# Kernel tuning notes

Hardware: AMD Instinct MI355X
Metric: run time of the kernel (lower is better)

## Reference

```python
import jax, jax.numpy as jnp
import numpy as np


def setup_inputs() -> dict:
    key = jax.random.key(0)
    k1, k2, k3 = jax.random.split(key, 3)
    x = jax.random.normal(k1, (32, 256, 32, 32), dtype=jnp.float32)
    weight = jax.random.normal(k2, (256, 256, 3, 3), dtype=jnp.float32) * 0.05
    bias = jax.random.normal(k3, (256,), dtype=jnp.float32) * 0.01
    return {"x": x, "weight": weight, "bias": bias}


def _forward(x, weight, bias):
    B, cin, n, _ = x.shape
    cout, _, k, _ = weight.shape
    s = (k - 1) // 2
    nf = n // 2 + 1
    bins = n * nf

    # fft shift matrix: exp(-1j*2*pi*s*(i+j)/n), kept rfft columns
    idx = jnp.arange(n)
    shift = idx[None, :] + idx[:, None]                     # (n, n)
    shift_m = jnp.exp(-1j * 2 * jnp.pi * s * shift / n)[:, :nf]
    shift_m = shift_m.reshape(bins, 1, 1).astype(jnp.complex64)

    # xfft: (B, cin, n, nf) -> (bins, cin, B)
    xfft = jnp.fft.rfft2(x)
    xfft = jnp.transpose(xfft, (2, 3, 1, 0)).reshape(bins, cin, B)

    # Hfft: (cout, cin, n, nf) -> (bins, cout, cin), shifted + conj
    Hfft = jnp.fft.rfft2(weight, s=(n, n)).reshape(cout, cin, bins)
    Hfft = shift_m * jnp.conj(jnp.transpose(Hfft, (2, 0, 1)))

    def sq_abs(z):
        return jnp.real(z) ** 2 + jnp.imag(z) ** 2

    RowNorm = jnp.sqrt(jnp.sum(sq_abs(Hfft), axis=2))       # (bins, cout)
    ColNorm = jnp.sqrt(jnp.sum(sq_abs(Hfft), axis=1))       # (bins, cin)

    if cout >= cin:
        RowLoss = jnp.mean((RowNorm - jnp.sqrt(cin / cout)) ** 2)
        ColLoss = jnp.mean((ColNorm - 1.0) ** 2)
        HHT = jnp.einsum('npc,nqc->npq', jnp.conj(Hfft), Hfft)  # (bins, cout, cout)
        mask = jnp.triu(jnp.ones((cout, cout), bool), k=1)
        count = bins * (cout * (cout - 1) // 2)
        AngLoss = jnp.sum(sq_abs(HHT) * mask[None]) / count   # MSE(|HHT[triu]|, 0)
        L = cout * ColLoss + cin * RowLoss + AngLoss
    else:
        RowLoss = jnp.mean((RowNorm - 1.0) ** 2)
        ColLoss = jnp.mean((ColNorm - jnp.sqrt(cout / cin)) ** 2)
        HTH = jnp.einsum('ndp,ndq->npq', jnp.conj(Hfft), Hfft)  # (bins, cin, cin)
        mask = jnp.triu(jnp.ones((cin, cin), bool), k=1)
        count = bins * (cin * (cin - 1) // 2)
        AngLoss = jnp.sum(sq_abs(HTH) * mask[None]) / count
        L = cout * ColLoss + cin * RowLoss + AngLoss

    # per-bin complex matmul: (bins, cout, cin) @ (bins, cin, B) -> (bins, cout, B)
    yfft = Hfft @ xfft
    yfft = jnp.transpose(yfft.reshape(n, nf, cout, B), (3, 2, 0, 1))  # (B, cout, n, nf)
    y = jnp.fft.irfft2(yfft, s=(n, n))
    y = y + bias[None, :, None, None]
    return y, L


def reference(x, weight, bias):
    return _forward(x, weight, bias)
```

## Files before the change

kernel.cpp:

```cpp
#include <hip/hip_runtime.h>
#include <math.h>

typedef __attribute__((ext_vector_type(8)))  short  short8;
typedef __attribute__((ext_vector_type(16))) float  float16;

#define TWO_PI_OVER_32 0.19634954084936207f

static __device__ __forceinline__ unsigned short f2bf(float f) {
    unsigned int u = __float_as_uint(f);
    u = (u + 0x7FFFu + ((u >> 16) & 1u)) >> 16;
    return (unsigned short)u;
}
static __device__ __forceinline__ float bf2f(unsigned short s) {
    return __uint_as_float(((unsigned int)s) << 16);
}

static __device__ __forceinline__ void g2l16(const void* g, void* l) {
    __builtin_amdgcn_global_load_lds(
        (const __attribute__((address_space(1))) unsigned int*)g,
        (__attribute__((address_space(3))) unsigned int*)l, 16, 0, 0);
}

__global__ __launch_bounds__(256) void k_prepx(const float* __restrict__ x,
                                               unsigned short* __restrict__ xb,
                                               const float* __restrict__ w,
                                               unsigned short* __restrict__ wt,
                                               unsigned short* __restrict__ Vb,
                                               float* __restrict__ Drow,
                                               float* __restrict__ Dcol,
                                               float* __restrict__ accum) {
    int tid = threadIdx.x;
    if (blockIdx.x < 4096) {
        int g = blockIdx.x * 256 + tid;
        int c = g & 31, r = (g >> 5) & 31, cig = (g >> 10) & 31, b = g >> 15;
        const float* xp = x + ((b * 256 + cig * 8) * 32 + r) * 32 + c;
        union { unsigned short u[8]; uint4 v; } pk;
        #pragma unroll
        for (int u = 0; u < 8; ++u) pk.u[u] = f2bf(xp[u * 1024]);
        ((uint4*)xb)[g] = pk.v;
        return;
    }
    __shared__ float sdata[45];
    __shared__ float ws2[256 * 9];
    int blk = blockIdx.x - 4096, lane = tid & 63;
    bool colmode = blk >= 256;
    int pc = blk & 255;
    if (blk == 0 && tid < 4) accum[tid] = 0.f;
    if (tid < 45) sdata[tid] = 0.f;

    int p = colmode ? tid : pc;
    int c = colmode ? pc : tid;
    float w9[9];
    #pragma unroll
    for (int t = 0; t < 9; ++t) w9[t] = w[(p * 256 + c) * 9 + t];
    if (!colmode) {
        #pragma unroll
        for (int t = 0; t < 9; ++t) ws2[tid * 9 + t] = w9[t];
    }
    __syncthreads();

    int idx = 0;
    for (int ta = 0; ta < 9; ++ta)
        for (int tb = ta; tb < 9; ++tb) {
            float v = w9[ta] * w9[tb];
            #pragma unroll
            for (int off = 32; off > 0; off >>= 1) v += __shfl_down(v, off);
            if (lane == 0) atomicAdd(&sdata[idx], v);
            ++idx;
        }
    __syncthreads();
    if (tid < 45) (colmode ? Dcol : Drow)[pc * 45 + tid] = sdata[tid];

    if (!colmode) {
        #pragma unroll
        for (int t = 0; t < 9; ++t)
            wt[t * 65536 + (c >> 3) * 2048 + p * 8 + (c & 7)] = f2bf(w9[t]);
        if (tid < 320) {
            int ta = tid >> 5, cig = tid & 31;
            union { unsigned short u[8]; uint4 v; } pk;
            #pragma unroll
            for (int u = 0; u < 8; ++u)
                pk.u[u] = (ta < 9) ? f2bf(ws2[(cig * 8 + u) * 9 + ta]) : (unsigned short)0;
            ((uint4*)Vb)[(p * 10 + ta) * 32 + cig] = pk.v;
        }
    }
}

__global__ __launch_bounds__(256, 2) void k_conv(const unsigned short* __restrict__ xb,
                                                 const unsigned short* __restrict__ wt,
                                                 const float* __restrict__ bias,
                                                 float* __restrict__ y) {
    __shared__ unsigned short wsm[2][1152 * 8];

    const int tid  = threadIdx.x;
    const int lane = tid & 63;
    const int wv   = tid >> 6;
    const int half = lane >> 5;
    const int m    = lane & 31;

    const int id    = blockIdx.x;
    const int xcd   = id & 7;
    const int local = id >> 3;
    const int b     = xcd * 4 + (local >> 4);
    const int rem   = local & 15;
    const int co0   = (rem & 3) * 64;
    const int r0    = (rem >> 2) * 8;

    float16 acc[2][2];
    #pragma unroll
    for (int i = 0; i < 2; ++i)
        #pragma unroll
        for (int ns = 0; ns < 2; ++ns)
            #pragma unroll
            for (int r = 0; r < 16; ++r) acc[i][ns][r] = 0.f;

    const uint4*  wtv = (const uint4*)wt;
    const short8* xbg = (const short8*)xb;

    auto stage = [&](int buf, int kc) {
        uint4* dst = (uint4*)wsm[buf];
        #pragma unroll
        for (int wc = wv; wc < 18; wc += 4) {
            int t = wc >> 1, cig = wc & 1;
            g2l16(&wtv[t * 8192 + (kc * 2 + cig) * 256 + co0 + lane],
                  &dst[wc * 64]);
        }
    };

    stage(0, 0);
    int cur = 0;

    #pragma unroll 1
    for (int kc = 0; kc < 16; ++kc) {
        __syncthreads();

        short8 bfr[4][3];
        {
            const long cb = ((long)(b * 32 + kc * 2 + half) * 32) * 32;
            #pragma unroll
            for (int s = 0; s < 4; ++s) {
                int gr = (r0 + wv * 2 + s + 31) & 31;
                #pragma unroll
                for (int btv = 0; btv < 3; ++btv)
                    bfr[s][btv] = xbg[cb + gr * 32 + ((m + btv + 31) & 31)];
            }
        }
        if (kc < 15) stage(cur ^ 1, kc + 1);

        const short8* wsl = (const short8*)wsm[cur];
        #pragma unroll
        for (int t = 0; t < 9; ++t) {
            const int atv = t / 3, btv = t % 3;
            short8 a0 = wsl[(t * 2 + half) * 64 + m];
            short8 a1 = wsl[(t * 2 + half) * 64 + 32 + m];
            #pragma unroll
            for (int ns = 0; ns < 2; ++ns) {
                acc[0][ns] = __builtin_amdgcn_mfma_f32_32x32x16_bf16(a0, bfr[ns + atv][btv], acc[0][ns], 0, 0, 0);
                acc[1][ns] = __builtin_amdgcn_mfma_f32_32x32x16_bf16(a1, bfr[ns + atv][btv], acc[1][ns], 0, 0, 0);
            }
        }
        cur ^= 1;
    }

    #pragma unroll
    for (int i = 0; i < 2; ++i) {
        #pragma unroll
        for (int ns = 0; ns < 2; ++ns) {
            int r = r0 + wv * 2 + ns;
            #pragma unroll
            for (int reg = 0; reg < 16; ++reg) {
                int crow = (reg & 3) + 8 * (reg >> 2) + 4 * half;
                int co = co0 + i * 32 + crow;
                y[(b * 256 + co) * 1024 + r * 32 + m] = acc[i][ns][reg] + bias[co];
            }
        }
    }
}

__global__ __launch_bounds__(256) void k_gram(const unsigned short* __restrict__ Vb,
                                              unsigned short* __restrict__ Gb) {
    int blk = blockIdx.x, I = 0;
    while (blk >= 20 - I) { blk -= 20 - I; ++I; }
    int J = I + blk;

    const int tid  = threadIdx.x;
    const int lane = tid & 63;
    const int wave = tid >> 6;
    const int wm = wave >> 1, wn = wave & 1;
    const int half = lane >> 5;
    const int m = lane & 31;

    const int row0 = I * 128 + wm * 64;
    const int col0 = J * 128 + wn * 64;

    float16 acc[2][2];
    #pragma unroll
    for (int i = 0; i < 2; ++i)
        #pragma unroll
        for (int j = 0; j < 2; ++j)
            #pragma unroll
            for (int r = 0; r < 16; ++r) acc[i][j][r] = 0.f;

    const short8* vb = (const short8*)Vb;
    for (int kc = 0; kc < 16; ++kc) {
        int cig = kc * 2 + half;
        short8 a0 = vb[(row0 + m) * 32 + cig];
        short8 a1 = vb[(row0 + 32 + m) * 32 + cig];
        short8 b0 = vb[(col0 + m) * 32 + cig];
        short8 b1 = vb[(col0 + 32 + m) * 32 + cig];
        acc[0][0] = __builtin_amdgcn_mfma_f32_32x32x16_bf16(a0, b0, acc[0][0], 0, 0, 0);
        acc[0][1] = __builtin_amdgcn_mfma_f32_32x32x16_bf16(a0, b1, acc[0][1], 0, 0, 0);
        acc[1][0] = __builtin_amdgcn_mfma_f32_32x32x16_bf16(a1, b0, acc[1][0], 0, 0, 0);
        acc[1][1] = __builtin_amdgcn_mfma_f32_32x32x16_bf16(a1, b1, acc[1][1], 0, 0, 0);
    }
    #pragma unroll
    for (int i = 0; i < 2; ++i)
        #pragma unroll
        for (int j = 0; j < 2; ++j)
            #pragma unroll
            for (int reg = 0; reg < 16; ++reg) {
                int crow = (reg & 3) + 8 * (reg >> 2) + 4 * half;
                Gb[(row0 + i * 32 + crow) * 2560 + col0 + j * 32 + m] =
                    f2bf(acc[i][j][reg]);
            }
}

__global__ __launch_bounds__(256) void k_loss(const float* __restrict__ Drow,
                                              const float* __restrict__ Dcol,
                                              const unsigned short* __restrict__ Gb,
                                              float* __restrict__ accum) {
    __shared__ union {
        struct { float coef[45]; float red[2]; } rc;
        struct { unsigned short gs[9 * 2560]; float red; } ang;
    } sh;
    int tid = threadIdx.x;

    if (blockIdx.x < 544) {
        int bin = blockIdx.x;
        int u = bin / 17, v = bin % 17;
        if (tid < 2) sh.rc.red[tid] = 0.f;
        if (tid < 45) {
            int idx = 0, TA = 0, TB = 0;
            for (int ta = 0; ta < 9; ++ta)
                for (int tb = ta; tb < 9; ++tb) {
                    if (idx == tid) { TA = ta; TB = tb; }
                    ++idx;
                }
            int da = TA / 3 - TB / 3;
            int db = TA % 3 - TB % 3;
            float cth = cosf(TWO_PI_OVER_32 * (float)(u * da + v * db));
            sh.rc.coef[tid] = (TA == TB) ? 1.f : 2.f * cth;
        }
        __syncthreads();

        float s1 = 0.f, s2 = 0.f;
        const float* dr = Drow + tid * 45;
        const float* dc = Dcol + tid * 45;
        #pragma unroll
        for (int i = 0; i < 45; ++i) {
            s1 += sh.rc.coef[i] * dr[i];
            s2 += sh.rc.coef[i] * dc[i];
        }
        float e1 = sqrtf(fmaxf(s1, 0.f)) - 1.f; e1 *= e1;
        float e2 = sqrtf(fmaxf(s2, 0.f)) - 1.f; e2 *= e2;
        #pragma unroll
        for (int off = 32; off > 0; off >>= 1) {
            e1 += __shfl_down(e1, off);
            e2 += __shfl_down(e2, off);
        }
        if ((tid & 63) == 0) { atomicAdd(&sh.rc.red[0], e1); atomicAdd(&sh.rc.red[1], e2); }
        __syncthreads();
        if (tid == 0) { atomicAdd(&accum[0], sh.rc.red[0]); atomicAdd(&accum[1], sh.rc.red[1]); }
    } else {
        int p = blockIdx.x - 544;
        if (tid == 0) sh.ang.red = 0.f;
        uint4* gsv = (uint4*)sh.ang.gs;
        const uint4* gbv = (const uint4*)Gb;
        for (int i = tid; i < 2880; i += 256) {
            int rr = i / 320, cc = i - rr * 320;
            gsv[i] = gbv[(p * 10 + rr) * 320 + cc];
        }
        __syncthreads();

        int q = tid;
        float S = 0.f;
        if (q > p) {
            float g5[5][5];
            #pragma unroll
            for (int i = 0; i < 5; ++i)
                #pragma unroll
                for (int j = 0; j < 5; ++j) g5[i][j] = 0.f;
            #pragma unroll
            for (int ta = 0; ta < 9; ++ta)
                #pragma unroll
                for (int tb = 0; tb < 9; ++tb) {
                    float c = bf2f(sh.ang.gs[ta * 2560 + q * 10 + tb]);
                    g5[ta / 3 - tb / 3 + 2][ta % 3 - tb % 3 + 2] += c;
                }
            float ReS[5];
            #pragma unroll
            for (int d = 0; d < 5; ++d) {
                float s = 0.f;
                for (int vv = 0; vv < 17; ++vv)
                    s += cosf(TWO_PI_OVER_32 * (float)(vv * d));
                ReS[d] = s;
            }
            #pragma unroll
            for (int da = 0; da < 5; ++da)
                #pragma unroll
                for (int d1 = 0; d1 < 5; ++d1)
                    #pragma unroll
                    for (int d2 = 0; d2 < 5; ++d2) {
                        int dd = d1 - d2; if (dd < 0) dd = -dd;
                        S += g5[da][d1] * g5[da][d2] * ReS[dd];
                    }
            S *= 32.f;
        }
        #pragma unroll
        for (int off = 32; off > 0; off >>= 1) S += __shfl_down(S, off);
        if ((tid & 63) == 0) atomicAdd(&sh.ang.red, S);
        __syncthreads();
        if (tid == 0) atomicAdd(&accum[2], sh.ang.red);
    }
}

__global__ void k_fin(const float* __restrict__ accum, float* __restrict__ out) {
    if (threadIdx.x == 0 && blockIdx.x == 0) {
        float row = accum[0], col = accum[1], ang = accum[2];
        out[8388608] = row / 544.f + col / 544.f + ang / (544.f * 32640.f);
    }
}

extern "C" void kernel_launch(void* const* d_in, const int* in_sizes, int n_in,
                              void* d_out, int out_size, void* d_ws, size_t ws_size,
                              hipStream_t stream) {
    const float* x    = (const float*)d_in[0];
    const float* w    = (const float*)d_in[1];
    const float* bias = (const float*)d_in[2];
    float* out = (float*)d_out;

    char* ws = (char*)d_ws;
    unsigned short* wt = (unsigned short*)ws;
    unsigned short* xb = (unsigned short*)(ws + 1179648);
    unsigned short* Gb = xb;
    unsigned short* Vb = (unsigned short*)(ws + 17956864);
    float* Drow  = (float*)(ws + 19267584);
    float* Dcol  = (float*)(ws + 19313664);
    float* accum = (float*)(ws + 19359744);

    k_prepx <<<4608, 256, 0, stream>>>(x, xb, w, wt, Vb, Drow, Dcol, accum);
    k_conv  <<<512, 256, 0, stream>>>(xb, wt, bias, out);
    k_gram  <<<210, 256, 0, stream>>>(Vb, Gb);
    k_loss  <<<800, 256, 0, stream>>>(Drow, Dcol, Gb, accum);
    k_fin   <<<1, 64, 0, stream>>>(accum, out);
}
```

Measured before the change: 179.0 us.

## Stage input tiles into LDS via async global_load_lds alongside weights

Input activation rows for each k-chunk are now staged into a double-buffered LDS region with async global-to-LDS loads, together with the weight tiles. This replaces the per-wave direct global loads into registers. The loop is unrolled by two with fixed buffer indices. The aim is to cut redundant global reads of overlapping rows across waves and overlap x loads with MFMA work, at the cost of extra LDS usage, which may reduce occupancy, and LDS reads inside the inner loop.

```diff
diff --git a/kernel.cpp b/kernel.cpp
--- a/kernel.cpp
+++ b/kernel.cpp
@@ -90,6 +90,7 @@
                                                  const unsigned short* __restrict__ wt,
                                                  const float* __restrict__ bias,
                                                  float* __restrict__ y) {
+    __shared__ unsigned short xs[2][640 * 8];
     __shared__ unsigned short wsm[2][1152 * 8];
 
     const int tid  = threadIdx.x;
@@ -114,40 +115,33 @@
             #pragma unroll
             for (int r = 0; r < 16; ++r) acc[i][ns][r] = 0.f;
 
-    const uint4*  wtv = (const uint4*)wt;
-    const short8* xbg = (const short8*)xb;
+    const uint4* xbv = (const uint4*)xb;
+    const uint4* wtv = (const uint4*)wt;
+
+    const int cigl = lane >> 5;
+    const int coll = lane & 31;
 
     auto stage = [&](int buf, int kc) {
-        uint4* dst = (uint4*)wsm[buf];
-        #pragma unroll
-        for (int wc = wv; wc < 18; wc += 4) {
-            int t = wc >> 1, cig = wc & 1;
-            g2l16(&wtv[t * 8192 + (kc * 2 + cig) * 256 + co0 + lane],
-                  &dst[wc * 64]);
+        uint4* xd = (uint4*)xs[buf];
+        uint4* wd = (uint4*)wsm[buf];
+        #pragma unroll
+        for (int ch = wv; ch < 28; ch += 4) {
+            if (ch < 10) {
+                int gr = (r0 + ch + 31) & 31;
+                g2l16(&xbv[((b * 32 + kc * 2 + cigl) * 32 + gr) * 32 + coll],
+                      &xd[ch * 64]);
+            } else {
+                int wc = ch - 10;
+                int t = wc >> 1, cig = wc & 1;
+                g2l16(&wtv[t * 8192 + (kc * 2 + cig) * 256 + co0 + lane],
+                      &wd[wc * 64]);
+            }
         }
     };
 
-    stage(0, 0);
-    int cur = 0;
-
-    #pragma unroll 1
-    for (int kc = 0; kc < 16; ++kc) {
-        __syncthreads();
-
-        short8 bfr[4][3];
-        {
-            const long cb = ((long)(b * 32 + kc * 2 + half) * 32) * 32;
-            #pragma unroll
-            for (int s = 0; s < 4; ++s) {
-                int gr = (r0 + wv * 2 + s + 31) & 31;
-                #pragma unroll
-                for (int btv = 0; btv < 3; ++btv)
-                    bfr[s][btv] = xbg[cb + gr * 32 + ((m + btv + 31) & 31)];
-            }
-        }
-        if (kc < 15) stage(cur ^ 1, kc + 1);
-
-        const short8* wsl = (const short8*)wsm[cur];
+    auto compute = [&](int buf) {
+        const short8* xsl = (const short8*)xs[buf];
+        const short8* wsl = (const short8*)wsm[buf];
         #pragma unroll
         for (int t = 0; t < 9; ++t) {
             const int atv = t / 3, btv = t % 3;
@@ -155,11 +149,23 @@
             short8 a1 = wsl[(t * 2 + half) * 64 + 32 + m];
             #pragma unroll
             for (int ns = 0; ns < 2; ++ns) {
-                acc[0][ns] = __builtin_amdgcn_mfma_f32_32x32x16_bf16(a0, bfr[ns + atv][btv], acc[0][ns], 0, 0, 0);
-                acc[1][ns] = __builtin_amdgcn_mfma_f32_32x32x16_bf16(a1, bfr[ns + atv][btv], acc[1][ns], 0, 0, 0);
-            }
-        }
-        cur ^= 1;
+                int slot = wv * 2 + ns + atv;
+                short8 bf = xsl[(slot * 2 + half) * 32 + ((m + btv + 31) & 31)];
+                acc[0][ns] = __builtin_amdgcn_mfma_f32_32x32x16_bf16(a0, bf, acc[0][ns], 0, 0, 0);
+                acc[1][ns] = __builtin_amdgcn_mfma_f32_32x32x16_bf16(a1, bf, acc[1][ns], 0, 0, 0);
+            }
+        }
+    };
+
+    stage(0, 0);
+    #pragma unroll 1
+    for (int kc2 = 0; kc2 < 8; ++kc2) {
+        __syncthreads();
+        stage(1, 2 * kc2 + 1);
+        compute(0);
+        __syncthreads();
+        if (kc2 < 7) stage(0, 2 * kc2 + 2);
+        compute(1);
     }
 
     #pragma unroll
```

Result: no change. 179.1 us (+0.1%).
